# Kernel optimization log

Hardware: AMD Instinct MI355X
Metric: run time of the kernel (lower is better)

## Reference

```python
import jax, jax.numpy as jnp
import numpy as np

N, D = 8192, 512
EPS = 1e-16

def setup_inputs() -> dict:
    key = jax.random.key(0)
    k1, k2, k3, k4 = jax.random.split(key, 4)
    user = jax.random.randint(k1, (N,), 0, 256, dtype=jnp.int32)
    timestamp = jax.random.uniform(k2, (N,), dtype=jnp.float32)
    is_click = jax.random.randint(k3, (N,), 0, 2) > 0  # bool [N]
    ad_embeddings = jax.random.normal(k4, (N, D), dtype=jnp.float32)
    return {"user": user, "timestamp": timestamp, "is_click": is_click,
            "ad_embeddings": ad_embeddings}

def reference(user, timestamp, is_click, ad_embeddings):
    # mask[i, j] = is_click[j] & (user[i] == user[j]) & (timestamp[i] > timestamp[j])
    user_matches = user[:, None] == user[None, :]              # [N, N]
    causal = timestamp[:, None] > timestamp[None, :]           # [N, N]
    mask = (is_click[None, :] & user_matches & causal).astype(ad_embeddings.dtype)
    norm_mask = mask / (mask.sum(axis=1, keepdims=True) + EPS)  # row-normalize
    history_emb = norm_mask @ ad_embeddings                     # [N, D]
    return history_emb
```

## Files before the change

kernel.cpp:

```cpp
#include <hip/hip_runtime.h>


constexpr int BLOCK   = 256;
constexpr int N_USERS = 256;
constexpr int CAP     = 1024;

__global__ void uht_detect_bool_layout(const unsigned char* __restrict__ clicks,
                                       int n, int* __restrict__ flag) {
    __shared__ int any;
    if (threadIdx.x == 0) any = 0;
    __syncthreads();
    int local = 0;
    for (int idx = threadIdx.x; idx < n; idx += blockDim.x) {
        if ((idx & 3) != 0 && clicks[idx] != 0) local = 1;
    }
    if (local) atomicOr(&any, 1);
    __syncthreads();
    if (threadIdx.x == 0) flag[0] = any;
}

template <int N_ROWS, int D_DIM>
__global__ __launch_bounds__(BLOCK)
void uht_user_walk_kernel(const int* __restrict__ user,
                          const float* __restrict__ ts,
                          const unsigned char* __restrict__ click_u8,
                          const float* __restrict__ emb,
                          float* __restrict__ out,
                          const int* __restrict__ layout_flag) {
    const int u = blockIdx.x;
    const int t = threadIdx.x;
    const bool bytewise = (layout_flag[0] != 0);
    const int* click_i32 = (const int*)click_u8;

    __shared__ int   mj[CAP];
    __shared__ float mts[CAP];
    __shared__ int   mclk[CAP];
    __shared__ int   sj[CAP];
    __shared__ float sts[CAP];
    __shared__ int   sclk[CAP];
    __shared__ int   cnt_lds;

    if (t == 0) cnt_lds = 0;
    __syncthreads();

    for (int j = t; j < N_ROWS; j += BLOCK) {
        if (user[j] == u) {
            const bool clicked = bytewise ? (click_u8[j] != 0)
                                          : (click_i32[j] != 0);
            int pos = atomicAdd(&cnt_lds, 1);
            if (pos < CAP) {
                mj[pos]   = j;
                mts[pos]  = ts[j];
                mclk[pos] = clicked ? 1 : 0;
            }
        }
    }
    __syncthreads();
    const int cnt = (cnt_lds < CAP) ? cnt_lds : CAP;

    for (int p = t; p < cnt; p += BLOCK) {
        const float tp = mts[p];
        const int   jp = mj[p];
        int r = 0;
        for (int q = 0; q < cnt; ++q) {
            const float tq = mts[q];
            r += (tq < tp || (tq == tp && mj[q] < jp)) ? 1 : 0;
        }
        sj[r]   = jp;
        sts[r]  = tp;
        sclk[r] = mclk[p];
    }
    __syncthreads();

    const float2* __restrict__ emb2 = (const float2*)emb;
    float2* __restrict__ out2 = (float2*)out;
    constexpr int D2 = D_DIM / 2;

    float2 S = make_float2(0.f, 0.f);
    int c = 0;
    int run_start = 0;

    for (int p = 0; p < cnt; ++p) {
        if (p > 0 && sts[p] != sts[p - 1]) {
            for (int q = run_start; q < p; ++q) {
                if (sclk[q]) {
                    const float2 e = emb2[(size_t)sj[q] * D2 + t];
                    S.x += e.x;
                    S.y += e.y;
                    ++c;
                }
            }
            run_start = p;
        }
        const float inv = 1.0f / ((float)c + 1e-16f);
        out2[(size_t)sj[p] * D2 + t] = make_float2(S.x * inv, S.y * inv);
    }
}

extern "C" void kernel_launch(void* const* d_in, const int* in_sizes, int n_in,
                              void* d_out, int out_size, void* d_ws, size_t ws_size,
                              hipStream_t stream) {
    const int* user = (const int*)d_in[0];
    const float* ts = (const float*)d_in[1];
    const unsigned char* clicks = (const unsigned char*)d_in[2];
    const float* emb = (const float*)d_in[3];
    float* out = (float*)d_out;
    int* flag = (int*)d_ws;

    const int n = in_sizes[0];
    (void)n_in; (void)out_size; (void)ws_size;

    uht_detect_bool_layout<<<1, BLOCK, 0, stream>>>(clicks, n, flag);
    uht_user_walk_kernel<8192, 512><<<N_USERS, BLOCK, 0, stream>>>(
        user, ts, clicks, emb, out, flag);
}
```

Baseline: 36.21 us.

## Fuse layout detection into per-user kernel and prefetch clicked embeddings into LDS

Removes the separate single-block layout-detection kernel. Each block now infers the bool layout itself from vectorized int4/float4/uchar4 loads of the full user, timestamp and click arrays. It precomputes, per row, how many clicks came strictly earlier and a compacted list of clicked rows, then bulk-prefetches up to 48 clicked embeddings into LDS. The final walk emits outputs by click count without the data-dependent run loop. CAP shrinks to 192, which assumes no user has more than 192 rows. Every block redundantly scans all inputs, and the dynamic LDS use rises to roughly 100KB per block, which limits occupancy.

```diff
diff --git a/kernel.cpp b/kernel.cpp
--- a/kernel.cpp
+++ b/kernel.cpp
@@ -3,97 +3,134 @@
 
 constexpr int BLOCK   = 256;
 constexpr int N_USERS = 256;
-constexpr int CAP     = 1024;
-
-__global__ void uht_detect_bool_layout(const unsigned char* __restrict__ clicks,
-                                       int n, int* __restrict__ flag) {
-    __shared__ int any;
-    if (threadIdx.x == 0) any = 0;
-    __syncthreads();
-    int local = 0;
-    for (int idx = threadIdx.x; idx < n; idx += blockDim.x) {
-        if ((idx & 3) != 0 && clicks[idx] != 0) local = 1;
-    }
-    if (local) atomicOr(&any, 1);
-    __syncthreads();
-    if (threadIdx.x == 0) flag[0] = any;
-}
+constexpr int CAP     = 192;
+constexpr int ECAP    = 48;
 
 template <int N_ROWS, int D_DIM>
 __global__ __launch_bounds__(BLOCK)
-void uht_user_walk_kernel(const int* __restrict__ user,
-                          const float* __restrict__ ts,
-                          const unsigned char* __restrict__ click_u8,
-                          const float* __restrict__ emb,
-                          float* __restrict__ out,
-                          const int* __restrict__ layout_flag) {
+void uht_fused_kernel(const int* __restrict__ user,
+                      const float* __restrict__ ts,
+                      const unsigned char* __restrict__ click_u8,
+                      const float* __restrict__ emb,
+                      float* __restrict__ out) {
+    constexpr int D2 = D_DIM / 2;
+    constexpr int G  = N_ROWS / (BLOCK * 4);
     const int u = blockIdx.x;
     const int t = threadIdx.x;
-    const bool bytewise = (layout_flag[0] != 0);
-    const int* click_i32 = (const int*)click_u8;
 
-    __shared__ int   mj[CAP];
-    __shared__ float mts[CAP];
-    __shared__ int   mclk[CAP];
-    __shared__ int   sj[CAP];
-    __shared__ float sts[CAP];
-    __shared__ int   sclk[CAP];
-    __shared__ int   cnt_lds;
+    extern __shared__ unsigned char smem[];
+    float2* elds = (float2*)smem;
+    int*    mj   = (int*)(smem + (size_t)ECAP * D2 * sizeof(float2));
+    float*  mts  = (float*)(mj + CAP);
+    int*    mclk = (int*)(mts + CAP);
+    int*    sj   = (int*)(mclk + CAP);
+    float*  sts  = (float*)(sj + CAP);
+    int*    sclk = (int*)(sts + CAP);
+    int*    cbef = (int*)(sclk + CAP);
+    int*    cljr = (int*)(cbef + CAP);
+    int*    misc = (int*)(cljr + CAP);
 
-    if (t == 0) cnt_lds = 0;
+    if (t == 0) { misc[0] = 0; misc[1] = 0; misc[2] = 0; }
     __syncthreads();
 
-    for (int j = t; j < N_ROWS; j += BLOCK) {
-        if (user[j] == u) {
-            const bool clicked = bytewise ? (click_u8[j] != 0)
-                                          : (click_i32[j] != 0);
-            int pos = atomicAdd(&cnt_lds, 1);
-            if (pos < CAP) {
-                mj[pos]   = j;
-                mts[pos]  = ts[j];
-                mclk[pos] = clicked ? 1 : 0;
+    const int4*   u4 = (const int4*)user;
+    const float4* t4 = (const float4*)ts;
+    const uchar4* c4 = (const uchar4*)click_u8;
+
+    int4 U[G]; float4 T[G]; uchar4 C[G];
+    bool nz = false;
+    #pragma unroll
+    for (int k = 0; k < G; ++k) {
+        const int idx = t + k * BLOCK;
+        U[k] = u4[idx];
+        T[k] = t4[idx];
+        C[k] = c4[idx];
+        nz = nz || (((int)C[k].y | (int)C[k].z | (int)C[k].w) != 0);
+    }
+    if (nz) atomicOr(&misc[1], 1);
+    __syncthreads();
+    const bool bytewise = (misc[1] != 0);
+
+    int4 CI[G];
+    if (!bytewise) {
+        const int4* ci4 = (const int4*)click_u8;
+        #pragma unroll
+        for (int k = 0; k < G; ++k) CI[k] = ci4[t + k * BLOCK];
+    }
+
+    #pragma unroll
+    for (int k = 0; k < G; ++k) {
+        const int base = 4 * (t + k * BLOCK);
+        const int   uu[4] = {U[k].x, U[k].y, U[k].z, U[k].w};
+        const float tt[4] = {T[k].x, T[k].y, T[k].z, T[k].w};
+        int cc[4];
+        if (bytewise) { cc[0] = C[k].x;  cc[1] = C[k].y;  cc[2] = C[k].z;  cc[3] = C[k].w; }
+        else          { cc[0] = CI[k].x; cc[1] = CI[k].y; cc[2] = CI[k].z; cc[3] = CI[k].w; }
+        #pragma unroll
+        for (int r = 0; r < 4; ++r) {
+            if (uu[r] == u) {
+                const int pos = atomicAdd(&misc[0], 1);
+                if (pos < CAP) {
+                    mj[pos]   = base + r;
+                    mts[pos]  = tt[r];
+                    mclk[pos] = (cc[r] != 0) ? 1 : 0;
+                }
             }
         }
     }
     __syncthreads();
-    const int cnt = (cnt_lds < CAP) ? cnt_lds : CAP;
+    const int cnt = min(misc[0], CAP);
 
-    for (int p = t; p < cnt; p += BLOCK) {
-        const float tp = mts[p];
-        const int   jp = mj[p];
+    if (t < cnt) {
+        const float tp = mts[t];
+        const int   jp = mj[t];
         int r = 0;
         for (int q = 0; q < cnt; ++q) {
             const float tq = mts[q];
             r += (tq < tp || (tq == tp && mj[q] < jp)) ? 1 : 0;
         }
-        sj[r]   = jp;
-        sts[r]  = tp;
-        sclk[r] = mclk[p];
+        sj[r] = jp; sts[r] = tp; sclk[r] = mclk[t];
     }
     __syncthreads();
 
+    if (t < cnt) {
+        const float tp = sts[t];
+        int cb = 0, pos = 0;
+        for (int q = 0; q < cnt; ++q) {
+            const int cq = sclk[q];
+            cb  += (cq && (sts[q] < tp)) ? 1 : 0;
+            pos += (cq && (q < t)) ? 1 : 0;
+        }
+        cbef[t] = cb;
+        if (sclk[t]) cljr[pos] = sj[t];
+        if (t == cnt - 1) misc[2] = pos + (sclk[t] ? 1 : 0);
+    }
+    __syncthreads();
+    const int nc  = misc[2];
+    const int ncs = min(nc, ECAP);
+
     const float2* __restrict__ emb2 = (const float2*)emb;
+    #pragma unroll 4
+    for (int m = 0; m < ncs; ++m) {
+        elds[m * D2 + t] = emb2[(size_t)cljr[m] * D2 + t];
+    }
+    __syncthreads();
+
     float2* __restrict__ out2 = (float2*)out;
-    constexpr int D2 = D_DIM / 2;
-
-    float2 S = make_float2(0.f, 0.f);
-    int c = 0;
-    int run_start = 0;
-
-    for (int p = 0; p < cnt; ++p) {
-        if (p > 0 && sts[p] != sts[p - 1]) {
-            for (int q = run_start; q < p; ++q) {
-                if (sclk[q]) {
-                    const float2 e = emb2[(size_t)sj[q] * D2 + t];
-                    S.x += e.x;
-                    S.y += e.y;
-                    ++c;
-                }
-            }
-            run_start = p;
+    float2 acc = make_float2(0.f, 0.f);
+    int p = 0;
+    for (int k = 0; ; ++k) {
+        const float inv = 1.0f / ((float)k + 1e-16f);
+        while (p < cnt && cbef[p] == k) {
+            out2[(size_t)sj[p] * D2 + t] = make_float2(acc.x * inv, acc.y * inv);
+            ++p;
         }
-        const float inv = 1.0f / ((float)c + 1e-16f);
-        out2[(size_t)sj[p] * D2 + t] = make_float2(S.x * inv, S.y * inv);
+        if (k >= nc) break;
+        float2 e;
+        if (k < ECAP) e = elds[k * D2 + t];
+        else          e = emb2[(size_t)cljr[k] * D2 + t];
+        acc.x += e.x;
+        acc.y += e.y;
     }
 }
 
@@ -105,12 +142,12 @@
     const unsigned char* clicks = (const unsigned char*)d_in[2];
     const float* emb = (const float*)d_in[3];
     float* out = (float*)d_out;
-    int* flag = (int*)d_ws;
+    (void)in_sizes; (void)n_in; (void)out_size; (void)d_ws; (void)ws_size;
 
-    const int n = in_sizes[0];
-    (void)n_in; (void)out_size; (void)ws_size;
-
-    uht_detect_bool_layout<<<1, BLOCK, 0, stream>>>(clicks, n, flag);
-    uht_user_walk_kernel<8192, 512><<<N_USERS, BLOCK, 0, stream>>>(
-        user, ts, clicks, emb, out, flag);
+    constexpr int D2 = 512 / 2;
+    const size_t shmem = (size_t)ECAP * D2 * sizeof(float2)
+                       + (size_t)8 * CAP * sizeof(int)
+                       + 16;
+    uht_fused_kernel<8192, 512><<<N_USERS, BLOCK, shmem, stream>>>(
+        user, ts, clicks, emb, out);
 }
```

After: 34.87 us. 3.7% less time.
